# Kernel optimization log

Hardware: AMD Instinct MI355X
Metric: run time of the kernel (lower is better)

Reference implementation:

```python
import jax, jax.numpy as jnp
import numpy as np

N_NODES_PER_GRAPH = 64
NUM_GRAPHS = 2048
N = NUM_GRAPHS * N_NODES_PER_GRAPH  # 131072 total nodes
E = N * 8                           # 1048576 edges
IN_DIM, H1, H2 = 64, 128, 64
OUT_DIM = (N_NODES_PER_GRAPH * N_NODES_PER_GRAPH - N_NODES_PER_GRAPH) // 2  # 2016


def setup_inputs() -> dict:
    key = jax.random.key(0)
    ks = jax.random.split(key, 16)
    s = 0.05
    x = jax.random.normal(ks[0], (N, IN_DIM), dtype=jnp.float32)
    # edges within each graph: offsets within graph + graph base offset
    src_local = jax.random.randint(ks[1], (E,), 0, N_NODES_PER_GRAPH)
    dst_local = jax.random.randint(ks[2], (E,), 0, N_NODES_PER_GRAPH)
    gid = jnp.repeat(jnp.arange(NUM_GRAPHS), E // NUM_GRAPHS) * N_NODES_PER_GRAPH
    edge_index = jnp.stack([src_local + gid, dst_local + gid]).astype(jnp.int64)
    batch = jnp.repeat(jnp.arange(NUM_GRAPHS), N_NODES_PER_GRAPH).astype(jnp.int64)
    eps = jax.random.normal(ks[3], (NUM_GRAPHS, H2), dtype=jnp.float32)
    return {
        "x": x, "edge_index": edge_index, "batch": batch, "eps": eps,
        "w1_rel": jax.random.normal(ks[4], (IN_DIM, H1)) * s,
        "b1": jnp.zeros((H1,), jnp.float32),
        "w1_root": jax.random.normal(ks[5], (IN_DIM, H1)) * s,
        "w2_rel": jax.random.normal(ks[6], (H1, H2)) * s,
        "b2": jnp.zeros((H2,), jnp.float32),
        "w2_root": jax.random.normal(ks[7], (H1, H2)) * s,
        "w3_rel": jax.random.normal(ks[8], (H1, H2)) * s,
        "b3": jnp.zeros((H2,), jnp.float32),
        "w3_root": jax.random.normal(ks[9], (H1, H2)) * s,
        "fc1_w": jax.random.normal(ks[10], (H2, H1)) * s,
        "fc1_b": jnp.zeros((H1,), jnp.float32),
        "fc2_w": jax.random.normal(ks[11], (H1, OUT_DIM)) * s,
        "fc2_b": jnp.zeros((OUT_DIM,), jnp.float32),
    }


def _graph_conv(h, src, dst, w_rel, b, w_root):
    # PyG GraphConv: out_i = W_rel @ (sum_{j in N(i)} h_j) + b + W_root @ h_i
    agg = jax.ops.segment_sum(h[src], dst, num_segments=N)  # [N, d_in]
    return agg @ w_rel + b + h @ w_root


def _segment_mean(h, seg):
    s = jax.ops.segment_sum(h, seg, num_segments=NUM_GRAPHS)
    cnt = jax.ops.segment_sum(jnp.ones((h.shape[0],), h.dtype), seg, num_segments=NUM_GRAPHS)
    return s / jnp.maximum(cnt, 1.0)[:, None]


def reference(x, edge_index, batch, eps, w1_rel, b1, w1_root, w2_rel, b2, w2_root,
              w3_rel, b3, w3_root, fc1_w, fc1_b, fc2_w, fc2_b):
    src, dst = edge_index[0], edge_index[1]
    # encode (dropout p=0.0 -> identity)
    h1 = jax.nn.relu(_graph_conv(x, src, dst, w1_rel, b1, w1_root))
    mu = _segment_mean(_graph_conv(h1, src, dst, w2_rel, b2, w2_root), batch)
    logvar = _segment_mean(_graph_conv(h1, src, dst, w3_rel, b3, w3_root), batch)
    # reparameterize with provided eps
    z = mu + eps * jnp.exp(0.5 * logvar)
    # decode
    h = jax.nn.relu(z @ fc1_w + fc1_b)
    recon = jax.nn.sigmoid(h @ fc2_w + fc2_b)
    return recon, mu, logvar
```

## Files before the change

kernel.cpp:

```cpp
#include <hip/hip_runtime.h>
#include <math.h>

#define NG 2048
#define NPG 64
#define EPG 512
#define ETOT (NG*EPG)
#define IND 64
#define H1D 128
#define H2D 64
#define OUTD 2016

typedef __attribute__((ext_vector_type(8))) short bf16x8;
typedef __attribute__((ext_vector_type(4))) float f32x4;

__device__ inline short f2b(float f) {
  union { float f; unsigned u; } v; v.f = f;
  unsigned r = (v.u + 0x7FFFu + ((v.u >> 16) & 1u)) >> 16;
  return (short)r;
}

__global__ void p_w1(const float* __restrict__ w1_rel, const float* __restrict__ w1_root,
                     short* __restrict__ WTg) {
  const int k = blockIdx.x;
  const int c = threadIdx.x;
  WTg[c*136 + k]      = f2b(w1_rel[k*H1D + c]);
  WTg[c*136 + 64 + k] = f2b(w1_root[k*H1D + c]);
}

__global__ __launch_bounds__(256, 4) void k1_encoder(
    const float* __restrict__ x, const int* __restrict__ ei,
    const short* __restrict__ WTg, const float* __restrict__ b1,
    short* __restrict__ SVg,
    const float* __restrict__ fc2_w, const float* __restrict__ w2_rel, const float* __restrict__ w2_root,
    const float* __restrict__ w3_rel, const float* __restrict__ w3_root,
    const float* __restrict__ fc1_w,
    short* __restrict__ WT2g, short* __restrict__ W23T, short* __restrict__ fc1T)
{
  __shared__ __align__(16) char smem[37632];
  const int g = blockIdx.x;
  const int tid = threadIdx.x;

  if (g >= NG) {
    float* L = (float*)smem;
    const int bid = g - NG;
    if (bid < 63) {
      const int c0 = bid*32;
      for (int i = tid; i < 4096; i += 256) {
        int k = i >> 5, c = i & 31;
        L[k*33 + c] = fc2_w[(size_t)k*OUTD + c0 + c];
      }
      __syncthreads();
      const int c = tid >> 3, k0 = (tid & 7)*16;
      for (int kk = 0; kk < 16; ++kk)
        WT2g[(size_t)(c0 + c)*136 + k0 + kk] = f2b(L[(k0 + kk)*33 + c]);
    } else if (bid < 67) {
      const int cc = bid - 63;
      const int j0 = cc*32;
      const float* wrel  = (cc < 2) ? w2_rel  : w3_rel;
      const float* wroot = (cc < 2) ? w2_root : w3_root;
      const int jl = j0 & 63;
      for (int i = tid; i < 4096; i += 256) {
        int k = i >> 5, c = i & 31;
        L[k*33 + c]        = wrel [k*H2D + jl + c];
        L[4224 + k*33 + c] = wroot[k*H2D + jl + c];
      }
      __syncthreads();
      const int c = tid >> 3, k0 = (tid & 7)*32;
      for (int kk = 0; kk < 32; ++kk) {
        int k = k0 + kk;
        float v = (k < 128) ? L[k*33 + c] : L[4224 + (k - 128)*33 + c];
        W23T[(size_t)(j0 + c)*264 + k] = f2b(v);
      }
    } else {
      const int c0 = (bid - 67)*64;
      for (int i = tid; i < 4096; i += 256) {
        int k = i >> 6, c = i & 63;
        L[k*65 + c] = fc1_w[k*H1D + c0 + c];
      }
      __syncthreads();
      const int c = tid >> 2, k0 = (tid & 3)*16;
      for (int kk = 0; kk < 16; ++kk)
        fc1T[(size_t)(c0 + c)*72 + k0 + kk] = f2b(L[(k0 + kk)*65 + c]);
    }
    return;
  }

  short* Xb    = (short*)smem;
  short* XbT   = (short*)(smem + 9216);
  float* Af    = (float*)(smem + 18432);
  float* dpart = (float*)(smem + 35328);
  float* deg   = (float*)(smem + 36352);
  float* hsum  = (float*)(smem + 36608);
  float* wsum  = (float*)(smem + 37120);

  const int w = tid >> 6, l = tid & 63;

  const int e0 = g*EPG + tid*2;
  const int s0 = ei[e0] & 63,     d0 = ei[ETOT + e0] & 63;
  const int s1 = ei[e0 + 1] & 63, d1 = ei[ETOT + e0 + 1] & 63;

  for (int i = tid; i < 64*66; i += 256) Af[i] = 0.f;
  if (tid < 128) { hsum[tid] = 0.f; wsum[tid] = 0.f; }

  {
    const int n = tid >> 2, f0 = (tid & 3) * 16;
    const float* xr = x + (size_t)g*(NPG*IND) + n*IND + f0;
    float4 v0 = *(const float4*)&xr[0];
    float4 v1 = *(const float4*)&xr[4];
    float4 v2 = *(const float4*)&xr[8];
    float4 v3 = *(const float4*)&xr[12];
    short b[16];
    b[0]=f2b(v0.x); b[1]=f2b(v0.y); b[2]=f2b(v0.z); b[3]=f2b(v0.w);
    b[4]=f2b(v1.x); b[5]=f2b(v1.y); b[6]=f2b(v1.z); b[7]=f2b(v1.w);
    b[8]=f2b(v2.x); b[9]=f2b(v2.y); b[10]=f2b(v2.z); b[11]=f2b(v2.w);
    b[12]=f2b(v3.x); b[13]=f2b(v3.y); b[14]=f2b(v3.z); b[15]=f2b(v3.w);
    short* xbp = &Xb[n*72 + f0];
    #pragma unroll
    for (int j = 0; j < 16; ++j) xbp[j] = b[j];
    #pragma unroll
    for (int j = 0; j < 16; ++j) XbT[(f0 + j)*72 + n] = b[j];
  }
  __syncthreads();

  atomicAdd(&Af[d0*66 + s0], 1.f);
  atomicAdd(&Af[d1*66 + s1], 1.f);
  __syncthreads();

  short cb[16];
  {
    const int scol = tid & 63, nrow0 = tid >> 6;
    float ps = 0.f;
    #pragma unroll
    for (int j = 0; j < 16; ++j) {
      float v = Af[(nrow0 + 4*j)*66 + scol];
      cb[j] = f2b(v); ps += v;
    }
    dpart[tid] = ps;
  }
  __syncthreads();

  short* Ab = (short*)Af;
  {
    const int scol = tid & 63, nrow0 = tid >> 6;
    #pragma unroll
    for (int j = 0; j < 16; ++j) Ab[(nrow0 + 4*j)*72 + scol] = cb[j];
  }
  if (tid < 64) deg[tid] = dpart[tid] + dpart[64 + tid] + dpart[128 + tid] + dpart[192 + tid];
  __syncthreads();

  const int rm = w*16;
  const int fr = l & 15;
  const int koff = (l >> 4) * 8;

  f32x4 agc[4];
  #pragma unroll
  for (int t = 0; t < 4; ++t) agc[t] = (f32x4){0.f,0.f,0.f,0.f};
  #pragma unroll
  for (int ks = 0; ks < 2; ++ks) {
    bf16x8 a = *(const bf16x8*)&Ab[(rm + fr)*72 + ks*32 + koff];
    #pragma unroll
    for (int t = 0; t < 4; ++t) {
      bf16x8 b = *(const bf16x8*)&XbT[(t*16 + fr)*72 + ks*32 + koff];
      agc[t] = __builtin_amdgcn_mfma_f32_16x16x32_bf16(a, b, agc[t], 0, 0, 0);
    }
  }
  __syncthreads();

  short* AGb = XbT;
  #pragma unroll
  for (int t = 0; t < 4; ++t)
    #pragma unroll
    for (int r = 0; r < 4; ++r)
      AGb[(rm + (l>>4)*4 + r)*72 + t*16 + fr] = f2b(agc[t][r]);
  __syncthreads();

  {
    float dg[4];
    #pragma unroll
    for (int r = 0; r < 4; ++r) dg[r] = deg[rm + (l>>4)*4 + r];

    f32x4 acc[8];
    #pragma unroll
    for (int t = 0; t < 8; ++t) acc[t] = (f32x4){0.f,0.f,0.f,0.f};
    #pragma unroll
    for (int ks = 0; ks < 4; ++ks) {
      bf16x8 a = (ks < 2)
        ? *(const bf16x8*)&AGb[(rm + fr)*72 + ks*32 + koff]
        : *(const bf16x8*)&Xb[(rm + fr)*72 + (ks-2)*32 + koff];
      #pragma unroll
      for (int t = 0; t < 8; ++t) {
        bf16x8 b = *(const bf16x8*)&WTg[(t*16 + fr)*136 + ks*32 + koff];
        acc[t] = __builtin_amdgcn_mfma_f32_16x16x32_bf16(a, b, acc[t], 0, 0, 0);
      }
    }
    #pragma unroll
    for (int t = 0; t < 8; ++t) {
      const int col = t*16 + fr;
      const float bb = b1[col];
      float hs = 0.f, ws = 0.f;
      #pragma unroll
      for (int r = 0; r < 4; ++r) {
        float v = fmaxf(acc[t][r] + bb, 0.f);
        hs += v; ws += dg[r]*v;
      }
      hs += __shfl_down(hs, 32); ws += __shfl_down(ws, 32);
      hs += __shfl_down(hs, 16); ws += __shfl_down(ws, 16);
      if (l < 16) { atomicAdd(&hsum[col], hs); atomicAdd(&wsum[col], ws); }
    }
  }
  __syncthreads();

  if (tid < 128) {
    SVg[(size_t)g*256 + tid]       = f2b(wsum[tid]);
    SVg[(size_t)g*256 + 128 + tid] = f2b(hsum[tid]);
  }
}

__global__ __launch_bounds__(256) void k1b_latent(
    const short* __restrict__ SVg, const short* __restrict__ W23T,
    const float* __restrict__ b2, const float* __restrict__ b3,
    const float* __restrict__ eps, const short* __restrict__ fc1T,
    const float* __restrict__ fc1_b,
    float* __restrict__ out_mu, float* __restrict__ out_lv, short* __restrict__ hbufB)
{
  __shared__ short SV[32*264];
  __shared__ short Zt[32*72];
  const int g0 = blockIdx.x * 32;
  const int tid = threadIdx.x;
  const int w = tid >> 6, l = tid & 63;
  const int s = w >> 1;
  const int h = w & 1;
  const int fr = l & 15;
  const int koff = (l >> 4) * 8;

  {
    const uint4* src = (const uint4*)(SVg + (size_t)g0*256);
    for (int i = tid; i < 1024; i += 256) {
      int r = i >> 5, k0 = (i & 31) * 8;
      *(uint4*)&SV[r*264 + k0] = src[i];
    }
  }
  __syncthreads();

  f32x4 acc[4];
  #pragma unroll
  for (int t = 0; t < 4; ++t) acc[t] = (f32x4){0.f,0.f,0.f,0.f};
  #pragma unroll
  for (int ks = 0; ks < 8; ++ks) {
    bf16x8 a = *(const bf16x8*)&SV[(s*16 + fr)*264 + ks*32 + koff];
    #pragma unroll
    for (int j = 0; j < 2; ++j) {
      bf16x8 bm = *(const bf16x8*)&W23T[((2*h + j)*16 + fr)*264 + ks*32 + koff];
      bf16x8 bl = *(const bf16x8*)&W23T[((2*h + j + 4)*16 + fr)*264 + ks*32 + koff];
      acc[j]     = __builtin_amdgcn_mfma_f32_16x16x32_bf16(a, bm, acc[j], 0, 0, 0);
      acc[2 + j] = __builtin_amdgcn_mfma_f32_16x16x32_bf16(a, bl, acc[2 + j], 0, 0, 0);
    }
  }
  #pragma unroll
  for (int j = 0; j < 2; ++j) {
    const int col = (2*h + j)*16 + fr;
    const float bb2 = b2[col], bb3 = b3[col];
    #pragma unroll
    for (int r = 0; r < 4; ++r) {
      const int row = s*16 + (l>>4)*4 + r;
      const size_t gg = (size_t)(g0 + row);
      float mu = acc[j][r]     * (1.f/64.f) + bb2;
      float lv = acc[2 + j][r] * (1.f/64.f) + bb3;
      out_mu[gg*64 + col] = mu;
      out_lv[gg*64 + col] = lv;
      float z = mu + eps[gg*64 + col] * __expf(0.5f*lv);
      Zt[row*72 + col] = f2b(z);
    }
  }
  __syncthreads();

  f32x4 hacc[4];
  #pragma unroll
  for (int t = 0; t < 4; ++t) hacc[t] = (f32x4){0.f,0.f,0.f,0.f};
  #pragma unroll
  for (int ks = 0; ks < 2; ++ks) {
    bf16x8 a = *(const bf16x8*)&Zt[(s*16 + fr)*72 + ks*32 + koff];
    #pragma unroll
    for (int j = 0; j < 4; ++j) {
      bf16x8 b = *(const bf16x8*)&fc1T[((h*4 + j)*16 + fr)*72 + ks*32 + koff];
      hacc[j] = __builtin_amdgcn_mfma_f32_16x16x32_bf16(a, b, hacc[j], 0, 0, 0);
    }
  }
  #pragma unroll
  for (int j = 0; j < 4; ++j) {
    const int col = (h*4 + j)*16 + fr;
    const float bb = fc1_b[col];
    #pragma unroll
    for (int r = 0; r < 4; ++r) {
      const int row = s*16 + (l>>4)*4 + r;
      hbufB[(size_t)(g0 + row)*H1D + col] = f2b(fmaxf(hacc[j][r] + bb, 0.f));
    }
  }
}

__global__ __launch_bounds__(256, 4) void k2_decoder(
    const short* __restrict__ hbufB, const short* __restrict__ WT2g,
    const float* __restrict__ fc2_b, float* __restrict__ recon)
{
  __shared__ __align__(16) short Hb[32*136];
  __shared__ __align__(16) short Wt[96*136];
  const int bx = blockIdx.x, by = blockIdx.y;
  const int tid = threadIdx.x;
  const int w = tid >> 6, l = tid & 63;

  {
    const uint4* src = (const uint4*)(hbufB + (size_t)bx*32*H1D);
    for (int i = tid; i < 512; i += 256) {
      int r = i >> 4, k0 = (i & 15) * 8;
      *(uint4*)&Hb[r*136 + k0] = src[i];
    }
  }
  {
    const uint4* src = (const uint4*)(WT2g + (size_t)by*96*136);
    uint4* dst = (uint4*)Wt;
    for (int i = tid; i < 1632; i += 256) dst[i] = src[i];
  }
  __syncthreads();

  const int s = w >> 1;
  const int h = w & 1;
  const int fr = l & 15;
  const int koff = (l >> 4) * 8;

  f32x4 acc[3];
  #pragma unroll
  for (int t = 0; t < 3; ++t) acc[t] = (f32x4){0.f,0.f,0.f,0.f};

  #pragma unroll
  for (int ks = 0; ks < 4; ++ks) {
    bf16x8 a = *(const bf16x8*)&Hb[(s*16 + fr)*136 + ks*32 + koff];
    #pragma unroll
    for (int t = 0; t < 3; ++t) {
      bf16x8 b = *(const bf16x8*)&Wt[(h*48 + t*16 + fr)*136 + ks*32 + koff];
      acc[t] = __builtin_amdgcn_mfma_f32_16x16x32_bf16(a, b, acc[t], 0, 0, 0);
    }
  }

  #pragma unroll
  for (int t = 0; t < 3; ++t) {
    const int col = by*96 + h*48 + t*16 + fr;
    const float bb = fc2_b[col];
    #pragma unroll
    for (int r = 0; r < 4; ++r) {
      const int row = bx*32 + s*16 + (l>>4)*4 + r;
      float v = acc[t][r] + bb;
      recon[(size_t)row*OUTD + col] = 1.f/(1.f + __expf(-v));
    }
  }
}

extern "C" void kernel_launch(void* const* d_in, const int* in_sizes, int n_in,
                              void* d_out, int out_size, void* d_ws, size_t ws_size,
                              hipStream_t stream) {
  const float* x       = (const float*)d_in[0];
  const int*   ei      = (const int*)d_in[1];
  const float* eps     = (const float*)d_in[3];
  const float* w1_rel  = (const float*)d_in[4];
  const float* b1      = (const float*)d_in[5];
  const float* w1_root = (const float*)d_in[6];
  const float* w2_rel  = (const float*)d_in[7];
  const float* b2      = (const float*)d_in[8];
  const float* w2_root = (const float*)d_in[9];
  const float* w3_rel  = (const float*)d_in[10];
  const float* b3      = (const float*)d_in[11];
  const float* w3_root = (const float*)d_in[12];
  const float* fc1_w   = (const float*)d_in[13];
  const float* fc1_b   = (const float*)d_in[14];
  const float* fc2_w   = (const float*)d_in[15];
  const float* fc2_b   = (const float*)d_in[16];

  float* recon  = (float*)d_out;
  float* out_mu = recon + (size_t)NG*OUTD;
  float* out_lv = out_mu + (size_t)NG*H2D;

  char* p = (char*)d_ws;
  short* WTg   = (short*)p;              p += 128*136*2;
  short* WT2g  = (short*)p;              p += 2016*136*2;
  short* fc1T  = (short*)p;              p += 128*72*2;
  short* W23T  = (short*)p;              p += 128*264*2;
  short* SVg   = (short*)p;              p += (size_t)NG*256*2;
  short* hbufB = (short*)p;

  p_w1<<<64, 128, 0, stream>>>(w1_rel, w1_root, WTg);
  k1_encoder<<<NG + 69, 256, 0, stream>>>(x, ei, WTg, b1, SVg,
      fc2_w, w2_rel, w2_root, w3_rel, w3_root, fc1_w, WT2g, W23T, fc1T);
  k1b_latent<<<64, 256, 0, stream>>>(SVg, W23T, b2, b3, eps, fc1T, fc1_b,
                                     out_mu, out_lv, hbufB);
  k2_decoder<<<dim3(64, 21), 256, 0, stream>>>(hbufB, WT2g, fc2_b, recon);
}
```

Before: 163.2 us.

## Pre-swizzle weights into MFMA fragment layout and pack adjacency counts as bytes

Measured after the change: 157.2 us. -3.7%, faster.

```diff
diff --git a/kernel.cpp b/kernel.cpp
--- a/kernel.cpp
+++ b/kernel.cpp
@@ -20,23 +20,31 @@
 }
 
 __global__ void p_w1(const float* __restrict__ w1_rel, const float* __restrict__ w1_root,
-                     short* __restrict__ WTg) {
-  const int k = blockIdx.x;
-  const int c = threadIdx.x;
-  WTg[c*136 + k]      = f2b(w1_rel[k*H1D + c]);
-  WTg[c*136 + 64 + k] = f2b(w1_root[k*H1D + c]);
-}
-
-__global__ __launch_bounds__(256, 4) void k1_encoder(
+                     short* __restrict__ WTgF) {
+  const int ct = blockIdx.x;
+  const int ks = threadIdx.x >> 6, l = threadIdx.x & 63;
+  const int col = ct*16 + (l & 15);
+  const int kb  = ks*32 + (l >> 4)*8;
+  short tmp[8];
+  #pragma unroll
+  for (int j = 0; j < 8; ++j) {
+    const int k = kb + j;
+    float v = (k < 64) ? w1_rel[k*H1D + col] : w1_root[(k - 64)*H1D + col];
+    tmp[j] = f2b(v);
+  }
+  *(uint4*)&WTgF[(size_t)((ct*4 + ks)*64 + l)*8] = *(uint4*)tmp;
+}
+
+__global__ __launch_bounds__(256, 3) void k1_encoder(
     const float* __restrict__ x, const int* __restrict__ ei,
-    const short* __restrict__ WTg, const float* __restrict__ b1,
+    const short* __restrict__ WTgF, const float* __restrict__ b1,
     short* __restrict__ SVg,
     const float* __restrict__ fc2_w, const float* __restrict__ w2_rel, const float* __restrict__ w2_root,
     const float* __restrict__ w3_rel, const float* __restrict__ w3_root,
     const float* __restrict__ fc1_w,
-    short* __restrict__ WT2g, short* __restrict__ W23T, short* __restrict__ fc1T)
+    short* __restrict__ WF2g, short* __restrict__ W23T, short* __restrict__ fc1T)
 {
-  __shared__ __align__(16) char smem[37632];
+  __shared__ __align__(16) char smem[42496];
   const int g = blockIdx.x;
   const int tid = threadIdx.x;
 
@@ -50,9 +58,21 @@
         L[k*33 + c] = fc2_w[(size_t)k*OUTD + c0 + c];
       }
       __syncthreads();
-      const int c = tid >> 3, k0 = (tid & 7)*16;
-      for (int kk = 0; kk < 16; ++kk)
-        WT2g[(size_t)(c0 + c)*136 + k0 + kk] = f2b(L[(k0 + kk)*33 + c]);
+      const int tl = tid >> 7;
+      const int r  = tid & 127;
+      const int ks = r >> 5;
+      const int lp = r & 31;
+      const int ct = bid*2 + tl;
+      #pragma unroll
+      for (int u = 0; u < 2; ++u) {
+        const int l = lp*2 + u;
+        const int cl = tl*16 + (l & 15);
+        const int kb = ks*32 + (l >> 4)*8;
+        short tmp[8];
+        #pragma unroll
+        for (int j = 0; j < 8; ++j) tmp[j] = f2b(L[(kb + j)*33 + cl]);
+        *(uint4*)&WF2g[(size_t)((ct*4 + ks)*64 + l)*8] = *(uint4*)tmp;
+      }
     } else if (bid < 67) {
       const int cc = bid - 63;
       const int j0 = cc*32;
@@ -85,13 +105,14 @@
     return;
   }
 
-  short* Xb    = (short*)smem;
-  short* XbT   = (short*)(smem + 9216);
-  float* Af    = (float*)(smem + 18432);
-  float* dpart = (float*)(smem + 35328);
-  float* deg   = (float*)(smem + 36352);
-  float* hsum  = (float*)(smem + 36608);
-  float* wsum  = (float*)(smem + 37120);
+  short* Xb   = (short*)smem;
+  short* XbT  = (short*)(smem + 9216);
+  short* Ab   = (short*)(smem + 18432);
+  unsigned* Au32 = (unsigned*)(smem + 27648);
+  short* AGb  = (short*)(smem + 32000);
+  float* deg  = (float*)(smem + 41216);
+  float* hsum = (float*)(smem + 41472);
+  float* wsum = (float*)(smem + 41984);
 
   const int w = tid >> 6, l = tid & 63;
 
@@ -99,7 +120,7 @@
   const int s0 = ei[e0] & 63,     d0 = ei[ETOT + e0] & 63;
   const int s1 = ei[e0 + 1] & 63, d1 = ei[ETOT + e0 + 1] & 63;
 
-  for (int i = tid; i < 64*66; i += 256) Af[i] = 0.f;
+  for (int i = tid; i < 64*17; i += 256) Au32[i] = 0u;
   if (tid < 128) { hsum[tid] = 0.f; wsum[tid] = 0.f; }
 
   {
@@ -122,30 +143,36 @@
   }
   __syncthreads();
 
-  atomicAdd(&Af[d0*66 + s0], 1.f);
-  atomicAdd(&Af[d1*66 + s1], 1.f);
-  __syncthreads();
-
-  short cb[16];
+  atomicAdd(&Au32[d0*17 + (s0 >> 2)], 1u << (8*(s0 & 3)));
+  atomicAdd(&Au32[d1*17 + (s1 >> 2)], 1u << (8*(s1 & 3)));
+  __syncthreads();
+
   {
-    const int scol = tid & 63, nrow0 = tid >> 6;
-    float ps = 0.f;
-    #pragma unroll
-    for (int j = 0; j < 16; ++j) {
-      float v = Af[(nrow0 + 4*j)*66 + scol];
-      cb[j] = f2b(v); ps += v;
-    }
-    dpart[tid] = ps;
-  }
-  __syncthreads();
-
-  short* Ab = (short*)Af;
-  {
-    const int scol = tid & 63, nrow0 = tid >> 6;
-    #pragma unroll
-    for (int j = 0; j < 16; ++j) Ab[(nrow0 + 4*j)*72 + scol] = cb[j];
-  }
-  if (tid < 64) deg[tid] = dpart[tid] + dpart[64 + tid] + dpart[128 + tid] + dpart[192 + tid];
+    const int row = tid >> 2, qw = tid & 3;
+    unsigned wds[4];
+    #pragma unroll
+    for (int q = 0; q < 4; ++q) wds[q] = Au32[row*17 + qw*4 + q];
+    unsigned* abp = (unsigned*)&Ab[row*72 + qw*16];
+    #pragma unroll
+    for (int q = 0; q < 4; ++q) {
+      unsigned wv = wds[q];
+      #pragma unroll
+      for (int p = 0; p < 2; ++p) {
+        unsigned c0 = (wv >> (16*p)) & 255u, c1 = (wv >> (16*p + 8)) & 255u;
+        abp[q*2 + p] = (unsigned)(unsigned short)f2b((float)c0)
+                     | ((unsigned)(unsigned short)f2b((float)c1) << 16);
+      }
+    }
+  }
+  if (tid < 16) {
+    unsigned s = 0;
+    #pragma unroll 8
+    for (int d = 0; d < 64; ++d) s += Au32[d*17 + tid];
+    deg[tid*4 + 0] = (float)(s & 255u);
+    deg[tid*4 + 1] = (float)((s >> 8) & 255u);
+    deg[tid*4 + 2] = (float)((s >> 16) & 255u);
+    deg[tid*4 + 3] = (float)(s >> 24);
+  }
   __syncthreads();
 
   const int rm = w*16;
@@ -164,35 +191,35 @@
       agc[t] = __builtin_amdgcn_mfma_f32_16x16x32_bf16(a, b, agc[t], 0, 0, 0);
     }
   }
-  __syncthreads();
-
-  short* AGb = XbT;
   #pragma unroll
   for (int t = 0; t < 4; ++t)
     #pragma unroll
     for (int r = 0; r < 4; ++r)
       AGb[(rm + (l>>4)*4 + r)*72 + t*16 + fr] = f2b(agc[t][r]);
-  __syncthreads();
 
   {
     float dg[4];
     #pragma unroll
     for (int r = 0; r < 4; ++r) dg[r] = deg[rm + (l>>4)*4 + r];
 
-    f32x4 acc[8];
-    #pragma unroll
-    for (int t = 0; t < 8; ++t) acc[t] = (f32x4){0.f,0.f,0.f,0.f};
-    #pragma unroll
-    for (int ks = 0; ks < 4; ++ks) {
-      bf16x8 a = (ks < 2)
+    bf16x8 afr[4];
+    #pragma unroll
+    for (int ks = 0; ks < 4; ++ks)
+      afr[ks] = (ks < 2)
         ? *(const bf16x8*)&AGb[(rm + fr)*72 + ks*32 + koff]
         : *(const bf16x8*)&Xb[(rm + fr)*72 + (ks-2)*32 + koff];
+
+    f32x4 acc[8];
+    #pragma unroll
+    for (int t = 0; t < 8; ++t) acc[t] = (f32x4){0.f,0.f,0.f,0.f};
+    #pragma unroll
+    for (int t = 0; t < 8; ++t)
       #pragma unroll
-      for (int t = 0; t < 8; ++t) {
-        bf16x8 b = *(const bf16x8*)&WTg[(t*16 + fr)*136 + ks*32 + koff];
-        acc[t] = __builtin_amdgcn_mfma_f32_16x16x32_bf16(a, b, acc[t], 0, 0, 0);
-      }
-    }
+      for (int ks = 0; ks < 4; ++ks) {
+        bf16x8 b = *(const bf16x8*)&WTgF[(size_t)((t*4 + ks)*64 + l)*8];
+        acc[t] = __builtin_amdgcn_mfma_f32_16x16x32_bf16(afr[ks], b, acc[t], 0, 0, 0);
+      }
+
     #pragma unroll
     for (int t = 0; t < 8; ++t) {
       const int col = t*16 + fr;
@@ -299,55 +326,48 @@
 }
 
 __global__ __launch_bounds__(256, 4) void k2_decoder(
-    const short* __restrict__ hbufB, const short* __restrict__ WT2g,
+    const short* __restrict__ hbufB, const short* __restrict__ WF2g,
     const float* __restrict__ fc2_b, float* __restrict__ recon)
 {
-  __shared__ __align__(16) short Hb[32*136];
-  __shared__ __align__(16) short Wt[96*136];
+  __shared__ __align__(16) short Hb[64*136];
   const int bx = blockIdx.x, by = blockIdx.y;
   const int tid = threadIdx.x;
   const int w = tid >> 6, l = tid & 63;
 
   {
-    const uint4* src = (const uint4*)(hbufB + (size_t)bx*32*H1D);
-    for (int i = tid; i < 512; i += 256) {
+    const uint4* src = (const uint4*)(hbufB + (size_t)bx*64*H1D);
+    for (int i = tid; i < 1024; i += 256) {
       int r = i >> 4, k0 = (i & 15) * 8;
       *(uint4*)&Hb[r*136 + k0] = src[i];
     }
   }
-  {
-    const uint4* src = (const uint4*)(WT2g + (size_t)by*96*136);
-    uint4* dst = (uint4*)Wt;
-    for (int i = tid; i < 1632; i += 256) dst[i] = src[i];
-  }
-  __syncthreads();
-
-  const int s = w >> 1;
-  const int h = w & 1;
+  __syncthreads();
+
   const int fr = l & 15;
   const int koff = (l >> 4) * 8;
 
-  f32x4 acc[3];
-  #pragma unroll
-  for (int t = 0; t < 3; ++t) acc[t] = (f32x4){0.f,0.f,0.f,0.f};
+  f32x4 acc[6];
+  #pragma unroll
+  for (int t = 0; t < 6; ++t) acc[t] = (f32x4){0.f,0.f,0.f,0.f};
 
   #pragma unroll
   for (int ks = 0; ks < 4; ++ks) {
-    bf16x8 a = *(const bf16x8*)&Hb[(s*16 + fr)*136 + ks*32 + koff];
-    #pragma unroll
-    for (int t = 0; t < 3; ++t) {
-      bf16x8 b = *(const bf16x8*)&Wt[(h*48 + t*16 + fr)*136 + ks*32 + koff];
+    bf16x8 a = *(const bf16x8*)&Hb[(w*16 + fr)*136 + ks*32 + koff];
+    #pragma unroll
+    for (int t = 0; t < 6; ++t) {
+      const int ct = by*6 + t;
+      bf16x8 b = *(const bf16x8*)&WF2g[(size_t)((ct*4 + ks)*64 + l)*8];
       acc[t] = __builtin_amdgcn_mfma_f32_16x16x32_bf16(a, b, acc[t], 0, 0, 0);
     }
   }
 
   #pragma unroll
-  for (int t = 0; t < 3; ++t) {
-    const int col = by*96 + h*48 + t*16 + fr;
+  for (int t = 0; t < 6; ++t) {
+    const int col = by*96 + t*16 + fr;
     const float bb = fc2_b[col];
     #pragma unroll
     for (int r = 0; r < 4; ++r) {
-      const int row = bx*32 + s*16 + (l>>4)*4 + r;
+      const int row = bx*64 + w*16 + (l>>4)*4 + r;
       float v = acc[t][r] + bb;
       recon[(size_t)row*OUTD + col] = 1.f/(1.f + __expf(-v));
     }
@@ -379,17 +399,17 @@
   float* out_lv = out_mu + (size_t)NG*H2D;
 
   char* p = (char*)d_ws;
-  short* WTg   = (short*)p;              p += 128*136*2;
-  short* WT2g  = (short*)p;              p += 2016*136*2;
+  short* WTgF  = (short*)p;              p += 8*4*64*8*2;
+  short* WF2g  = (short*)p;              p += 126*4*64*8*2;
   short* fc1T  = (short*)p;              p += 128*72*2;
   short* W23T  = (short*)p;              p += 128*264*2;
   short* SVg   = (short*)p;              p += (size_t)NG*256*2;
   short* hbufB = (short*)p;
 
-  p_w1<<<64, 128, 0, stream>>>(w1_rel, w1_root, WTg);
-  k1_encoder<<<NG + 69, 256, 0, stream>>>(x, ei, WTg, b1, SVg,
-      fc2_w, w2_rel, w2_root, w3_rel, w3_root, fc1_w, WT2g, W23T, fc1T);
+  p_w1<<<8, 256, 0, stream>>>(w1_rel, w1_root, WTgF);
+  k1_encoder<<<NG + 69, 256, 0, stream>>>(x, ei, WTgF, b1, SVg,
+      fc2_w, w2_rel, w2_root, w3_rel, w3_root, fc1_w, WF2g, W23T, fc1T);
   k1b_latent<<<64, 256, 0, stream>>>(SVg, W23T, b2, b3, eps, fc1T, fc1_b,
                                      out_mu, out_lv, hbufB);
-  k2_decoder<<<dim3(64, 21), 256, 0, stream>>>(hbufB, WT2g, fc2_b, recon);
-}
+  k2_decoder<<<dim3(32, 21), 256, 0, stream>>>(hbufB, WF2g, fc2_b, recon);
+}
```
